# Kernel optimization log

Hardware: AMD Instinct MI355X
Metric: run time of the kernel (lower is better)

The kernel has to match this reference:

```python
import jax, jax.numpy as jnp
import numpy as np

C = 256
H_CH = 128  # channels // 2 (stage_index != 2)


def _gelu(x):
    # torch nn.GELU() default: exact erf formulation
    return jax.nn.gelu(x, approximate=False)


def _ln_channels(x, gamma, beta):
    # LayerNorm over channel dim (axis=1) of NCHW, eps=1e-5 (torch default)
    mu = jnp.mean(x, axis=1, keepdims=True)
    var = jnp.var(x, axis=1, keepdims=True)
    xn = (x - mu) * jax.lax.rsqrt(var + 1e-5)
    return xn * gamma[None, :, None, None] + beta[None, :, None, None]


def setup_inputs() -> dict:
    key = jax.random.key(0)
    ks = jax.random.split(key, 9)
    x = jax.random.normal(ks[0], (16, C, 64, 64), dtype=jnp.float32)
    s1 = 1.0 / np.sqrt(C)
    s2 = 1.0 / np.sqrt(H_CH)
    W1 = jax.random.uniform(ks[1], (H_CH, C), jnp.float32, -s1, s1)
    b1 = jax.random.uniform(ks[2], (H_CH,), jnp.float32, -s1, s1)
    g1 = jnp.ones((H_CH,), jnp.float32)
    be1 = jnp.zeros((H_CH,), jnp.float32)
    W2 = jax.random.uniform(ks[3], (C, H_CH), jnp.float32, -s2, s2)
    b2 = jax.random.uniform(ks[4], (C,), jnp.float32, -s2, s2)
    g2 = jnp.ones((C,), jnp.float32)
    be2 = jnp.zeros((C,), jnp.float32)
    return {"x": x, "W1": W1, "b1": b1, "g1": g1, "be1": be1,
            "W2": W2, "b2": b2, "g2": g2, "be2": be2}


def reference(x, W1, b1, g1, be1, W2, b2, g2, be2):
    identity = x
    # 1x1 conv == per-pixel channel matmul
    h = jnp.einsum('bchw,oc->bohw', x, W1) + b1[None, :, None, None]
    h = _gelu(_ln_channels(h, g1, be1))
    y = jnp.einsum('bchw,oc->bohw', h, W2) + b2[None, :, None, None]
    y = _ln_channels(y, g2, be2)
    return _gelu(y + identity)
```

## Files before the change

kernel.cpp:

```cpp
#include <hip/hip_runtime.h>

#define C_IN 256
#define HC   128
#define HW   4096

#define SX 260
#define SH 132
#define SO 68

typedef __attribute__((ext_vector_type(8))) short short8;
typedef __attribute__((ext_vector_type(4))) short short4v;
typedef __attribute__((ext_vector_type(4))) float f32x4;
typedef __attribute__((ext_vector_type(4))) unsigned short u16x4;

__device__ __forceinline__ unsigned short f2bf(float f) {
    union { float f; unsigned int u; } v; v.f = f;
    return (unsigned short)((v.u + 0x7FFFu + ((v.u >> 16) & 1u)) >> 16);
}

__device__ __forceinline__ float gelu_f(float v) {
    const float u = v * (0.7978845608028654f + 0.035677408136300125f * v * v);
    const float e = __expf(2.0f * u);
    const float t = 1.0f - 2.0f * __builtin_amdgcn_rcpf(e + 1.0f);
    return 0.5f * v * (1.0f + t);
}

__global__ void convert_weights(const float* __restrict__ W1, const float* __restrict__ W2,
                                unsigned short* __restrict__ W1b, unsigned short* __restrict__ W2b) {
    int i = blockIdx.x * blockDim.x + threadIdx.x;
    if (i < HC * C_IN) { W1b[i] = f2bf(W1[i]); W2b[i] = f2bf(W2[i]); }
}

union SmemU {
    unsigned short Xs[64 * SX];
    struct { unsigned short Hs[64 * SH]; float Ob[4][16][SO]; } u2;
};

template<bool USE_WS>
__global__ __launch_bounds__(256, 4) void fused_mlp(
    const float* __restrict__ x,
    const float* __restrict__ W1, const float* __restrict__ b1,
    const float* __restrict__ g1, const float* __restrict__ be1,
    const float* __restrict__ W2, const float* __restrict__ b2,
    const float* __restrict__ g2, const float* __restrict__ be2,
    const unsigned short* __restrict__ W1b, const unsigned short* __restrict__ W2b,
    float* __restrict__ out)
{
    __shared__ alignas(16) SmemU sm;
    __shared__ float red[4][64][2];

    const int tid = threadIdx.x;
    const int wv  = tid >> 6;
    const int l   = tid & 63;
    const int l15 = l & 15;
    const int kg  = l >> 4;

    const int tile = blockIdx.x;
    const int b    = tile >> 6;
    const int p0   = (tile & 63) * 64;
    const float* xb = x   + (size_t)b * (C_IN * HW) + p0;
    float*       ob = out + (size_t)b * (C_IN * HW) + p0;

    {
        const int g  = l15;
        const int cr = kg;
        #pragma unroll
        for (int rnd = 0; rnd < 4; ++rnd) {
            const int c0 = rnd * 64 + wv * 16 + cr * 4;
            f32x4 v[4];
            #pragma unroll
            for (int j = 0; j < 4; ++j)
                v[j] = *reinterpret_cast<const f32x4*>(xb + (size_t)(c0 + j) * HW + g * 4);
            #pragma unroll
            for (int jj = 0; jj < 4; ++jj) {
                u16x4 pk;
                #pragma unroll
                for (int j = 0; j < 4; ++j) pk[j] = f2bf(v[j][jj]);
                *reinterpret_cast<u16x4*>(&sm.Xs[(size_t)(g * 4 + jj) * SX + c0]) = pk;
            }
        }
    }
    __syncthreads();

    f32x4 acc1[2][4];
    const f32x4 vzero = {0.f, 0.f, 0.f, 0.f};
    #pragma unroll
    for (int mt = 0; mt < 2; ++mt)
        #pragma unroll
        for (int nt = 0; nt < 4; ++nt) acc1[mt][nt] = vzero;

    const int r0 = wv * 32;
    #pragma unroll
    for (int ks = 0; ks < 8; ++ks) {
        const int kb = ks * 32 + kg * 8;
        short8 a[2]; short4v blo[4], bhi[4];
        #pragma unroll
        for (int mt = 0; mt < 2; ++mt) {
            const int row = r0 + mt * 16 + l15;
            if constexpr (USE_WS) {
                a[mt] = *reinterpret_cast<const short8*>(W1b + (size_t)row * C_IN + kb);
            } else {
                const float* wp = W1 + (size_t)row * C_IN + kb;
                const f32x4 f0 = *reinterpret_cast<const f32x4*>(wp);
                const f32x4 f1 = *reinterpret_cast<const f32x4*>(wp + 4);
                #pragma unroll
                for (int e = 0; e < 4; ++e) { a[mt][e] = (short)f2bf(f0[e]); a[mt][4+e] = (short)f2bf(f1[e]); }
            }
        }
        #pragma unroll
        for (int nt = 0; nt < 4; ++nt) {
            const unsigned short* p = &sm.Xs[(size_t)(nt * 16 + l15) * SX + kb];
            blo[nt] = *reinterpret_cast<const short4v*>(p);
            bhi[nt] = *reinterpret_cast<const short4v*>(p + 4);
        }
        #pragma unroll
        for (int mt = 0; mt < 2; ++mt)
            #pragma unroll
            for (int nt = 0; nt < 4; ++nt) {
                const short8 bf = __builtin_shufflevector(blo[nt], bhi[nt], 0,1,2,3,4,5,6,7);
                acc1[mt][nt] = __builtin_amdgcn_mfma_f32_16x16x32_bf16(a[mt], bf, acc1[mt][nt], 0, 0, 0);
            }
    }

    #pragma unroll
    for (int mt = 0; mt < 2; ++mt) {
        const f32x4 bias = *reinterpret_cast<const f32x4*>(b1 + r0 + mt * 16 + kg * 4);
        #pragma unroll
        for (int nt = 0; nt < 4; ++nt) acc1[mt][nt] += bias;
    }
    #pragma unroll
    for (int nt = 0; nt < 4; ++nt) {
        float s = 0.f, q = 0.f;
        #pragma unroll
        for (int mt = 0; mt < 2; ++mt)
            #pragma unroll
            for (int r = 0; r < 4; ++r) { const float v = acc1[mt][nt][r]; s += v; q += v * v; }
        s += __shfl_xor(s, 16); s += __shfl_xor(s, 32);
        q += __shfl_xor(q, 16); q += __shfl_xor(q, 32);
        if (kg == 0) { red[wv][nt * 16 + l15][0] = s; red[wv][nt * 16 + l15][1] = q; }
    }
    __syncthreads();

    {
        f32x4 gm[2], bt[2];
        #pragma unroll
        for (int mt = 0; mt < 2; ++mt) {
            gm[mt] = *reinterpret_cast<const f32x4*>(g1  + r0 + mt * 16 + kg * 4);
            bt[mt] = *reinterpret_cast<const f32x4*>(be1 + r0 + mt * 16 + kg * 4);
        }
        #pragma unroll
        for (int nt = 0; nt < 4; ++nt) {
            const int col = nt * 16 + l15;
            float s = 0.f, q = 0.f;
            #pragma unroll
            for (int w2 = 0; w2 < 4; ++w2) { s += red[w2][col][0]; q += red[w2][col][1]; }
            const float mean = s * (1.0f / HC);
            const float rstd = rsqrtf(q * (1.0f / HC) - mean * mean + 1e-5f);
            #pragma unroll
            for (int mt = 0; mt < 2; ++mt) {
                u16x4 pk;
                #pragma unroll
                for (int r = 0; r < 4; ++r) {
                    float v = (acc1[mt][nt][r] - mean) * rstd;
                    v = v * gm[mt][r] + bt[mt][r];
                    pk[r] = f2bf(gelu_f(v));
                }
                *reinterpret_cast<u16x4*>(&sm.u2.Hs[(size_t)col * SH + r0 + mt * 16 + kg * 4]) = pk;
            }
        }
    }
    __syncthreads();

    f32x4 acc2[4][4];
    #pragma unroll
    for (int mt = 0; mt < 4; ++mt)
        #pragma unroll
        for (int nt = 0; nt < 4; ++nt) acc2[mt][nt] = vzero;

    const int r2 = wv * 64;
    #pragma unroll
    for (int ks = 0; ks < 4; ++ks) {
        const int kb = ks * 32 + kg * 8;
        short8 a[4]; short4v blo[4], bhi[4];
        #pragma unroll
        for (int mt = 0; mt < 4; ++mt) {
            const int row = r2 + mt * 16 + l15;
            if constexpr (USE_WS) {
                a[mt] = *reinterpret_cast<const short8*>(W2b + (size_t)row * HC + kb);
            } else {
                const float* wp = W2 + (size_t)row * HC + kb;
                const f32x4 f0 = *reinterpret_cast<const f32x4*>(wp);
                const f32x4 f1 = *reinterpret_cast<const f32x4*>(wp + 4);
                #pragma unroll
                for (int e = 0; e < 4; ++e) { a[mt][e] = (short)f2bf(f0[e]); a[mt][4+e] = (short)f2bf(f1[e]); }
            }
        }
        #pragma unroll
        for (int nt = 0; nt < 4; ++nt) {
            const unsigned short* p = &sm.u2.Hs[(size_t)(nt * 16 + l15) * SH + kb];
            blo[nt] = *reinterpret_cast<const short4v*>(p);
            bhi[nt] = *reinterpret_cast<const short4v*>(p + 4);
        }
        #pragma unroll
        for (int mt = 0; mt < 4; ++mt)
            #pragma unroll
            for (int nt = 0; nt < 4; ++nt) {
                const short8 bf = __builtin_shufflevector(blo[nt], bhi[nt], 0,1,2,3,4,5,6,7);
                acc2[mt][nt] = __builtin_amdgcn_mfma_f32_16x16x32_bf16(a[mt], bf, acc2[mt][nt], 0, 0, 0);
            }
    }

    #pragma unroll
    for (int mt = 0; mt < 4; ++mt) {
        const f32x4 bias = *reinterpret_cast<const f32x4*>(b2 + r2 + mt * 16 + kg * 4);
        #pragma unroll
        for (int nt = 0; nt < 4; ++nt) acc2[mt][nt] += bias;
    }
    #pragma unroll
    for (int nt = 0; nt < 4; ++nt) {
        float s = 0.f, q = 0.f;
        #pragma unroll
        for (int mt = 0; mt < 4; ++mt)
            #pragma unroll
            for (int r = 0; r < 4; ++r) { const float v = acc2[mt][nt][r]; s += v; q += v * v; }
        s += __shfl_xor(s, 16); s += __shfl_xor(s, 32);
        q += __shfl_xor(q, 16); q += __shfl_xor(q, 32);
        if (kg == 0) { red[wv][nt * 16 + l15][0] = s; red[wv][nt * 16 + l15][1] = q; }
    }
    __syncthreads();

    float mean2[4], rstd2[4];
    #pragma unroll
    for (int nt = 0; nt < 4; ++nt) {
        const int col = nt * 16 + l15;
        float s = 0.f, q = 0.f;
        #pragma unroll
        for (int w2 = 0; w2 < 4; ++w2) { s += red[w2][col][0]; q += red[w2][col][1]; }
        mean2[nt] = s * (1.0f / C_IN);
        rstd2[nt] = rsqrtf(q * (1.0f / C_IN) - mean2[nt] * mean2[nt] + 1e-5f);
    }

    #pragma unroll
    for (int mt = 0; mt < 4; ++mt) {
        const f32x4 gm = *reinterpret_cast<const f32x4*>(g2  + r2 + mt * 16 + kg * 4);
        const f32x4 bt = *reinterpret_cast<const f32x4*>(be2 + r2 + mt * 16 + kg * 4);
        #pragma unroll
        for (int nt = 0; nt < 4; ++nt) {
            #pragma unroll
            for (int r = 0; r < 4; ++r) {
                float v = (acc2[mt][nt][r] - mean2[nt]) * rstd2[nt];
                v = v * gm[r] + bt[r];
                sm.u2.Ob[wv][kg * 4 + r][nt * 16 + l15] = v;
            }
        }
        __syncthreads();
        #pragma unroll
        for (int m = 0; m < 4; ++m) {
            const int rl  = kg + 4 * m;
            const int row = r2 + mt * 16 + rl;
            const f32x4 y4 = *reinterpret_cast<const f32x4*>(&sm.u2.Ob[wv][rl][l15 * 4]);
            const f32x4 x4 = *reinterpret_cast<const f32x4*>(xb + (size_t)row * HW + l15 * 4);
            f32x4 o4;
            #pragma unroll
            for (int e = 0; e < 4; ++e) o4[e] = gelu_f(y4[e] + x4[e]);
            *reinterpret_cast<f32x4*>(ob + (size_t)row * HW + l15 * 4) = o4;
        }
        if (mt < 3) __syncthreads();
    }
}

extern "C" void kernel_launch(void* const* d_in, const int* in_sizes, int n_in,
                              void* d_out, int out_size, void* d_ws, size_t ws_size,
                              hipStream_t stream) {
    const float* x   = (const float*)d_in[0];
    const float* W1  = (const float*)d_in[1];
    const float* b1  = (const float*)d_in[2];
    const float* g1  = (const float*)d_in[3];
    const float* be1 = (const float*)d_in[4];
    const float* W2  = (const float*)d_in[5];
    const float* b2  = (const float*)d_in[6];
    const float* g2  = (const float*)d_in[7];
    const float* be2 = (const float*)d_in[8];
    float* out = (float*)d_out;

    const size_t need = (size_t)(HC * C_IN + C_IN * HC) * sizeof(unsigned short);
    if (ws_size >= need) {
        unsigned short* W1b = (unsigned short*)d_ws;
        unsigned short* W2b = W1b + HC * C_IN;
        convert_weights<<<128, 256, 0, stream>>>(W1, W2, W1b, W2b);
        fused_mlp<true><<<1024, 256, 0, stream>>>(x, W1, b1, g1, be1, W2, b2, g2, be2, W1b, W2b, out);
    } else {
        fused_mlp<false><<<1024, 256, 0, stream>>>(x, W1, b1, g1, be1, W2, b2, g2, be2, nullptr, nullptr, out);
    }
}
```

Measured before the change: 58.98 us.

## Halve pixel tile to 32, double grid, use per-wave LDS fences in epilogue

Shrinks each block's pixel tile from 64 to 32, doubling the grid to 2048 blocks and raising the launch-bounds occupancy target from 4 to 8 blocks per CU. LDS and accumulator register use drop accordingly. The second GEMM now loads W2 fragments in two halves to reduce live registers. The epilogue's block-wide barriers are replaced with wave-local LDS waitcnt fences, since each wave only touches its own Ob slice. The trade-off is that each W1/W2 fragment loaded is reused across half as many pixels, so per-pixel weight traffic rises.

```diff
diff --git a/kernel.cpp b/kernel.cpp
--- a/kernel.cpp
+++ b/kernel.cpp
@@ -3,10 +3,11 @@
 #define C_IN 256
 #define HC   128
 #define HW   4096
+#define TP   32
 
 #define SX 260
 #define SH 132
-#define SO 68
+#define SO 36
 
 typedef __attribute__((ext_vector_type(8))) short short8;
 typedef __attribute__((ext_vector_type(4))) short short4v;
@@ -25,6 +26,11 @@
     return 0.5f * v * (1.0f + t);
 }
 
+__device__ __forceinline__ void wave_lds_fence() {
+    asm volatile("s_waitcnt lgkmcnt(0)" ::: "memory");
+    __builtin_amdgcn_sched_barrier(0);
+}
+
 __global__ void convert_weights(const float* __restrict__ W1, const float* __restrict__ W2,
                                 unsigned short* __restrict__ W1b, unsigned short* __restrict__ W2b) {
     int i = blockIdx.x * blockDim.x + threadIdx.x;
@@ -32,12 +38,12 @@
 }
 
 union SmemU {
-    unsigned short Xs[64 * SX];
-    struct { unsigned short Hs[64 * SH]; float Ob[4][16][SO]; } u2;
+    unsigned short Xs[TP * SX];
+    struct { unsigned short Hs[TP * SH]; float Ob[4][16][SO]; } u2;
 };
 
 template<bool USE_WS>
-__global__ __launch_bounds__(256, 4) void fused_mlp(
+__global__ __launch_bounds__(256, 8) void fused_mlp(
     const float* __restrict__ x,
     const float* __restrict__ W1, const float* __restrict__ b1,
     const float* __restrict__ g1, const float* __restrict__ be1,
@@ -47,7 +53,7 @@
     float* __restrict__ out)
 {
     __shared__ alignas(16) SmemU sm;
-    __shared__ float red[4][64][2];
+    __shared__ float red[4][TP][2];
 
     const int tid = threadIdx.x;
     const int wv  = tid >> 6;
@@ -56,17 +62,17 @@
     const int kg  = l >> 4;
 
     const int tile = blockIdx.x;
-    const int b    = tile >> 6;
-    const int p0   = (tile & 63) * 64;
+    const int b    = tile >> 7;
+    const int p0   = (tile & 127) * TP;
     const float* xb = x   + (size_t)b * (C_IN * HW) + p0;
     float*       ob = out + (size_t)b * (C_IN * HW) + p0;
 
     {
-        const int g  = l15;
-        const int cr = kg;
-        #pragma unroll
-        for (int rnd = 0; rnd < 4; ++rnd) {
-            const int c0 = rnd * 64 + wv * 16 + cr * 4;
+        const int g  = tid & 7;
+        const int cq = tid >> 3;
+        #pragma unroll
+        for (int rnd = 0; rnd < 2; ++rnd) {
+            const int c0 = rnd * 128 + cq * 4;
             f32x4 v[4];
             #pragma unroll
             for (int j = 0; j < 4; ++j)
@@ -82,18 +88,18 @@
     }
     __syncthreads();
 
-    f32x4 acc1[2][4];
+    f32x4 acc1[2][2];
     const f32x4 vzero = {0.f, 0.f, 0.f, 0.f};
     #pragma unroll
     for (int mt = 0; mt < 2; ++mt)
         #pragma unroll
-        for (int nt = 0; nt < 4; ++nt) acc1[mt][nt] = vzero;
+        for (int nt = 0; nt < 2; ++nt) acc1[mt][nt] = vzero;
 
     const int r0 = wv * 32;
     #pragma unroll
     for (int ks = 0; ks < 8; ++ks) {
         const int kb = ks * 32 + kg * 8;
-        short8 a[2]; short4v blo[4], bhi[4];
+        short8 a[2]; short4v blo[2], bhi[2];
         #pragma unroll
         for (int mt = 0; mt < 2; ++mt) {
             const int row = r0 + mt * 16 + l15;
@@ -108,7 +114,7 @@
             }
         }
         #pragma unroll
-        for (int nt = 0; nt < 4; ++nt) {
+        for (int nt = 0; nt < 2; ++nt) {
             const unsigned short* p = &sm.Xs[(size_t)(nt * 16 + l15) * SX + kb];
             blo[nt] = *reinterpret_cast<const short4v*>(p);
             bhi[nt] = *reinterpret_cast<const short4v*>(p + 4);
@@ -116,7 +122,7 @@
         #pragma unroll
         for (int mt = 0; mt < 2; ++mt)
             #pragma unroll
-            for (int nt = 0; nt < 4; ++nt) {
+            for (int nt = 0; nt < 2; ++nt) {
                 const short8 bf = __builtin_shufflevector(blo[nt], bhi[nt], 0,1,2,3,4,5,6,7);
                 acc1[mt][nt] = __builtin_amdgcn_mfma_f32_16x16x32_bf16(a[mt], bf, acc1[mt][nt], 0, 0, 0);
             }
@@ -126,10 +132,10 @@
     for (int mt = 0; mt < 2; ++mt) {
         const f32x4 bias = *reinterpret_cast<const f32x4*>(b1 + r0 + mt * 16 + kg * 4);
         #pragma unroll
-        for (int nt = 0; nt < 4; ++nt) acc1[mt][nt] += bias;
-    }
-    #pragma unroll
-    for (int nt = 0; nt < 4; ++nt) {
+        for (int nt = 0; nt < 2; ++nt) acc1[mt][nt] += bias;
+    }
+    #pragma unroll
+    for (int nt = 0; nt < 2; ++nt) {
         float s = 0.f, q = 0.f;
         #pragma unroll
         for (int mt = 0; mt < 2; ++mt)
@@ -149,7 +155,7 @@
             bt[mt] = *reinterpret_cast<const f32x4*>(be1 + r0 + mt * 16 + kg * 4);
         }
         #pragma unroll
-        for (int nt = 0; nt < 4; ++nt) {
+        for (int nt = 0; nt < 2; ++nt) {
             const int col = nt * 16 + l15;
             float s = 0.f, q = 0.f;
             #pragma unroll
@@ -171,53 +177,57 @@
     }
     __syncthreads();
 
-    f32x4 acc2[4][4];
+    f32x4 acc2[4][2];
     #pragma unroll
     for (int mt = 0; mt < 4; ++mt)
         #pragma unroll
-        for (int nt = 0; nt < 4; ++nt) acc2[mt][nt] = vzero;
+        for (int nt = 0; nt < 2; ++nt) acc2[mt][nt] = vzero;
 
     const int r2 = wv * 64;
     #pragma unroll
     for (int ks = 0; ks < 4; ++ks) {
         const int kb = ks * 32 + kg * 8;
-        short8 a[4]; short4v blo[4], bhi[4];
-        #pragma unroll
-        for (int mt = 0; mt < 4; ++mt) {
-            const int row = r2 + mt * 16 + l15;
-            if constexpr (USE_WS) {
-                a[mt] = *reinterpret_cast<const short8*>(W2b + (size_t)row * HC + kb);
-            } else {
-                const float* wp = W2 + (size_t)row * HC + kb;
-                const f32x4 f0 = *reinterpret_cast<const f32x4*>(wp);
-                const f32x4 f1 = *reinterpret_cast<const f32x4*>(wp + 4);
-                #pragma unroll
-                for (int e = 0; e < 4; ++e) { a[mt][e] = (short)f2bf(f0[e]); a[mt][4+e] = (short)f2bf(f1[e]); }
-            }
-        }
-        #pragma unroll
-        for (int nt = 0; nt < 4; ++nt) {
+        short4v blo[2], bhi[2];
+        #pragma unroll
+        for (int nt = 0; nt < 2; ++nt) {
             const unsigned short* p = &sm.u2.Hs[(size_t)(nt * 16 + l15) * SH + kb];
             blo[nt] = *reinterpret_cast<const short4v*>(p);
             bhi[nt] = *reinterpret_cast<const short4v*>(p + 4);
         }
         #pragma unroll
-        for (int mt = 0; mt < 4; ++mt)
-            #pragma unroll
-            for (int nt = 0; nt < 4; ++nt) {
-                const short8 bf = __builtin_shufflevector(blo[nt], bhi[nt], 0,1,2,3,4,5,6,7);
-                acc2[mt][nt] = __builtin_amdgcn_mfma_f32_16x16x32_bf16(a[mt], bf, acc2[mt][nt], 0, 0, 0);
-            }
+        for (int half = 0; half < 2; ++half) {
+            short8 a[2];
+            #pragma unroll
+            for (int m2 = 0; m2 < 2; ++m2) {
+                const int row = r2 + (half * 2 + m2) * 16 + l15;
+                if constexpr (USE_WS) {
+                    a[m2] = *reinterpret_cast<const short8*>(W2b + (size_t)row * HC + kb);
+                } else {
+                    const float* wp = W2 + (size_t)row * HC + kb;
+                    const f32x4 f0 = *reinterpret_cast<const f32x4*>(wp);
+                    const f32x4 f1 = *reinterpret_cast<const f32x4*>(wp + 4);
+                    #pragma unroll
+                    for (int e = 0; e < 4; ++e) { a[m2][e] = (short)f2bf(f0[e]); a[m2][4+e] = (short)f2bf(f1[e]); }
+                }
+            }
+            #pragma unroll
+            for (int m2 = 0; m2 < 2; ++m2)
+                #pragma unroll
+                for (int nt = 0; nt < 2; ++nt) {
+                    const short8 bf = __builtin_shufflevector(blo[nt], bhi[nt], 0,1,2,3,4,5,6,7);
+                    acc2[half * 2 + m2][nt] = __builtin_amdgcn_mfma_f32_16x16x32_bf16(a[m2], bf, acc2[half * 2 + m2][nt], 0, 0, 0);
+                }
+        }
     }
 
     #pragma unroll
     for (int mt = 0; mt < 4; ++mt) {
         const f32x4 bias = *reinterpret_cast<const f32x4*>(b2 + r2 + mt * 16 + kg * 4);
         #pragma unroll
-        for (int nt = 0; nt < 4; ++nt) acc2[mt][nt] += bias;
-    }
-    #pragma unroll
-    for (int nt = 0; nt < 4; ++nt) {
+        for (int nt = 0; nt < 2; ++nt) acc2[mt][nt] += bias;
+    }
+    #pragma unroll
+    for (int nt = 0; nt < 2; ++nt) {
         float s = 0.f, q = 0.f;
         #pragma unroll
         for (int mt = 0; mt < 4; ++mt)
@@ -229,9 +239,9 @@
     }
     __syncthreads();
 
-    float mean2[4], rstd2[4];
-    #pragma unroll
-    for (int nt = 0; nt < 4; ++nt) {
+    float mean2[2], rstd2[2];
+    #pragma unroll
+    for (int nt = 0; nt < 2; ++nt) {
         const int col = nt * 16 + l15;
         float s = 0.f, q = 0.f;
         #pragma unroll
@@ -245,7 +255,7 @@
         const f32x4 gm = *reinterpret_cast<const f32x4*>(g2  + r2 + mt * 16 + kg * 4);
         const f32x4 bt = *reinterpret_cast<const f32x4*>(be2 + r2 + mt * 16 + kg * 4);
         #pragma unroll
-        for (int nt = 0; nt < 4; ++nt) {
+        for (int nt = 0; nt < 2; ++nt) {
             #pragma unroll
             for (int r = 0; r < 4; ++r) {
                 float v = (acc2[mt][nt][r] - mean2[nt]) * rstd2[nt];
@@ -253,19 +263,20 @@
                 sm.u2.Ob[wv][kg * 4 + r][nt * 16 + l15] = v;
             }
         }
-        __syncthreads();
-        #pragma unroll
-        for (int m = 0; m < 4; ++m) {
-            const int rl  = kg + 4 * m;
+        wave_lds_fence();
+        #pragma unroll
+        for (int m = 0; m < 2; ++m) {
+            const int rl  = (l >> 3) + 8 * m;
+            const int cq4 = (l & 7) * 4;
             const int row = r2 + mt * 16 + rl;
-            const f32x4 y4 = *reinterpret_cast<const f32x4*>(&sm.u2.Ob[wv][rl][l15 * 4]);
-            const f32x4 x4 = *reinterpret_cast<const f32x4*>(xb + (size_t)row * HW + l15 * 4);
+            const f32x4 y4 = *reinterpret_cast<const f32x4*>(&sm.u2.Ob[wv][rl][cq4]);
+            const f32x4 x4 = *reinterpret_cast<const f32x4*>(xb + (size_t)row * HW + cq4);
             f32x4 o4;
             #pragma unroll
             for (int e = 0; e < 4; ++e) o4[e] = gelu_f(y4[e] + x4[e]);
-            *reinterpret_cast<f32x4*>(ob + (size_t)row * HW + l15 * 4) = o4;
-        }
-        if (mt < 3) __syncthreads();
+            *reinterpret_cast<f32x4*>(ob + (size_t)row * HW + cq4) = o4;
+        }
+        if (mt < 3) wave_lds_fence();
     }
 }
 
@@ -288,8 +299,8 @@
         unsigned short* W1b = (unsigned short*)d_ws;
         unsigned short* W2b = W1b + HC * C_IN;
         convert_weights<<<128, 256, 0, stream>>>(W1, W2, W1b, W2b);
-        fused_mlp<true><<<1024, 256, 0, stream>>>(x, W1, b1, g1, be1, W2, b2, g2, be2, W1b, W2b, out);
+        fused_mlp<true><<<2048, 256, 0, stream>>>(x, W1, b1, g1, be1, W2, b2, g2, be2, W1b, W2b, out);
     } else {
-        fused_mlp<false><<<1024, 256, 0, stream>>>(x, W1, b1, g1, be1, W2, b2, g2, be2, nullptr, nullptr, out);
-    }
-}
+        fused_mlp<false><<<2048, 256, 0, stream>>>(x, W1, b1, g1, be1, W2, b2, g2, be2, nullptr, nullptr, out);
+    }
+}
```

Result: slower. 69.68 us (+18.1%).

## Split x staging across GEMM1 halves, prefetch residual, replace block barriers with wave fences

Applied to the files above, without the earlier changes.

The x tile load is split so the second half of channels is loaded early and converted to LDS after the first half of GEMM1, overlapping global loads with MFMA work. Residual x rows for the epilogue are prefetched before GEMM2 and one step ahead in each epilogue iteration. The per-wave output staging buffer now uses only an lgkmcnt wait instead of a full __syncthreads, since each wave owns its own slice. W2 fragment loads are split into halves to reduce register pressure, and gelu switches to exp2f. Holding more data in registers may raise VGPR use and lower occupancy.

```diff
diff --git a/kernel.cpp b/kernel.cpp
--- a/kernel.cpp
+++ b/kernel.cpp
@@ -3,6 +3,7 @@
 #define C_IN 256
 #define HC   128
 #define HW   4096
+#define TP   64
 
 #define SX 260
 #define SH 132
@@ -11,6 +12,7 @@
 typedef __attribute__((ext_vector_type(8))) short short8;
 typedef __attribute__((ext_vector_type(4))) short short4v;
 typedef __attribute__((ext_vector_type(4))) float f32x4;
+typedef __attribute__((ext_vector_type(2))) float f32x2;
 typedef __attribute__((ext_vector_type(4))) unsigned short u16x4;
 
 __device__ __forceinline__ unsigned short f2bf(float f) {
@@ -20,9 +22,20 @@
 
 __device__ __forceinline__ float gelu_f(float v) {
     const float u = v * (0.7978845608028654f + 0.035677408136300125f * v * v);
-    const float e = __expf(2.0f * u);
+    const float e = exp2f(u * 2.8853900817779268f);
     const float t = 1.0f - 2.0f * __builtin_amdgcn_rcpf(e + 1.0f);
     return 0.5f * v * (1.0f + t);
+}
+
+__device__ __forceinline__ void block_sync() {
+    asm volatile("s_waitcnt lgkmcnt(0)" ::: "memory");
+    __builtin_amdgcn_s_barrier();
+    asm volatile("" ::: "memory");
+    __builtin_amdgcn_sched_barrier(0);
+}
+
+__device__ __forceinline__ void wave_lds_fence() {
+    asm volatile("s_waitcnt lgkmcnt(0)" ::: "memory");
 }
 
 __global__ void convert_weights(const float* __restrict__ W1, const float* __restrict__ W2,
@@ -32,8 +45,8 @@
 }
 
 union SmemU {
-    unsigned short Xs[64 * SX];
-    struct { unsigned short Hs[64 * SH]; float Ob[4][16][SO]; } u2;
+    unsigned short Xs[TP * SX];
+    struct { unsigned short Hs[TP * SH]; float Ob[4][16][SO]; } u2;
 };
 
 template<bool USE_WS>
@@ -47,7 +60,7 @@
     float* __restrict__ out)
 {
     __shared__ alignas(16) SmemU sm;
-    __shared__ float red[4][64][2];
+    __shared__ float red[4][TP][2];
 
     const int tid = threadIdx.x;
     const int wv  = tid >> 6;
@@ -55,32 +68,37 @@
     const int l15 = l & 15;
     const int kg  = l >> 4;
 
-    const int tile = blockIdx.x;
-    const int b    = tile >> 6;
-    const int p0   = (tile & 63) * 64;
+    const int bid = blockIdx.x;
+    const int b   = bid >> 6;
+    const int p0  = (bid & 63) * TP;
     const float* xb = x   + (size_t)b * (C_IN * HW) + p0;
     float*       ob = out + (size_t)b * (C_IN * HW) + p0;
 
-    {
-        const int g  = l15;
-        const int cr = kg;
-        #pragma unroll
-        for (int rnd = 0; rnd < 4; ++rnd) {
-            const int c0 = rnd * 64 + wv * 16 + cr * 4;
-            f32x4 v[4];
-            #pragma unroll
-            for (int j = 0; j < 4; ++j)
-                v[j] = *reinterpret_cast<const f32x4*>(xb + (size_t)(c0 + j) * HW + g * 4);
-            #pragma unroll
-            for (int jj = 0; jj < 4; ++jj) {
-                u16x4 pk;
-                #pragma unroll
-                for (int j = 0; j < 4; ++j) pk[j] = f2bf(v[j][jj]);
-                *reinterpret_cast<u16x4*>(&sm.Xs[(size_t)(g * 4 + jj) * SX + c0]) = pk;
-            }
-        }
-    }
-    __syncthreads();
+    const int g  = l15;
+    const int cs = wv * 16 + kg * 4;
+    f32x4 v0[8], v1[8];
+    #pragma unroll
+    for (int rnd = 0; rnd < 2; ++rnd)
+        #pragma unroll
+        for (int j = 0; j < 4; ++j)
+            v0[rnd * 4 + j] = *reinterpret_cast<const f32x4*>(xb + (size_t)(rnd * 64 + cs + j) * HW + g * 4);
+    #pragma unroll
+    for (int rnd = 0; rnd < 2; ++rnd)
+        #pragma unroll
+        for (int j = 0; j < 4; ++j)
+            v1[rnd * 4 + j] = *reinterpret_cast<const f32x4*>(xb + (size_t)((rnd + 2) * 64 + cs + j) * HW + g * 4);
+    #pragma unroll
+    for (int rnd = 0; rnd < 2; ++rnd) {
+        const int c0 = rnd * 64 + cs;
+        #pragma unroll
+        for (int jj = 0; jj < 4; ++jj) {
+            u16x4 pk;
+            #pragma unroll
+            for (int j = 0; j < 4; ++j) pk[j] = f2bf(v0[rnd * 4 + j][jj]);
+            *reinterpret_cast<u16x4*>(&sm.Xs[(size_t)(g * 4 + jj) * SX + c0]) = pk;
+        }
+    }
+    block_sync();
 
     f32x4 acc1[2][4];
     const f32x4 vzero = {0.f, 0.f, 0.f, 0.f};
@@ -91,7 +109,7 @@
 
     const int r0 = wv * 32;
     #pragma unroll
-    for (int ks = 0; ks < 8; ++ks) {
+    for (int ks = 0; ks < 4; ++ks) {
         const int kb = ks * 32 + kg * 8;
         short8 a[2]; short4v blo[4], bhi[4];
         #pragma unroll
@@ -123,6 +141,51 @@
     }
 
     #pragma unroll
+    for (int rnd = 0; rnd < 2; ++rnd) {
+        const int c0 = (rnd + 2) * 64 + cs;
+        #pragma unroll
+        for (int jj = 0; jj < 4; ++jj) {
+            u16x4 pk;
+            #pragma unroll
+            for (int j = 0; j < 4; ++j) pk[j] = f2bf(v1[rnd * 4 + j][jj]);
+            *reinterpret_cast<u16x4*>(&sm.Xs[(size_t)(g * 4 + jj) * SX + c0]) = pk;
+        }
+    }
+    block_sync();
+
+    #pragma unroll
+    for (int ks = 4; ks < 8; ++ks) {
+        const int kb = ks * 32 + kg * 8;
+        short8 a[2]; short4v blo[4], bhi[4];
+        #pragma unroll
+        for (int mt = 0; mt < 2; ++mt) {
+            const int row = r0 + mt * 16 + l15;
+            if constexpr (USE_WS) {
+                a[mt] = *reinterpret_cast<const short8*>(W1b + (size_t)row * C_IN + kb);
+            } else {
+                const float* wp = W1 + (size_t)row * C_IN + kb;
+                const f32x4 f0 = *reinterpret_cast<const f32x4*>(wp);
+                const f32x4 f1 = *reinterpret_cast<const f32x4*>(wp + 4);
+                #pragma unroll
+                for (int e = 0; e < 4; ++e) { a[mt][e] = (short)f2bf(f0[e]); a[mt][4+e] = (short)f2bf(f1[e]); }
+            }
+        }
+        #pragma unroll
+        for (int nt = 0; nt < 4; ++nt) {
+            const unsigned short* p = &sm.Xs[(size_t)(nt * 16 + l15) * SX + kb];
+            blo[nt] = *reinterpret_cast<const short4v*>(p);
+            bhi[nt] = *reinterpret_cast<const short4v*>(p + 4);
+        }
+        #pragma unroll
+        for (int mt = 0; mt < 2; ++mt)
+            #pragma unroll
+            for (int nt = 0; nt < 4; ++nt) {
+                const short8 bf = __builtin_shufflevector(blo[nt], bhi[nt], 0,1,2,3,4,5,6,7);
+                acc1[mt][nt] = __builtin_amdgcn_mfma_f32_16x16x32_bf16(a[mt], bf, acc1[mt][nt], 0, 0, 0);
+            }
+    }
+
+    #pragma unroll
     for (int mt = 0; mt < 2; ++mt) {
         const f32x4 bias = *reinterpret_cast<const f32x4*>(b1 + r0 + mt * 16 + kg * 4);
         #pragma unroll
@@ -139,7 +202,7 @@
         q += __shfl_xor(q, 16); q += __shfl_xor(q, 32);
         if (kg == 0) { red[wv][nt * 16 + l15][0] = s; red[wv][nt * 16 + l15][1] = q; }
     }
-    __syncthreads();
+    block_sync();
 
     {
         f32x4 gm[2], bt[2];
@@ -169,7 +232,13 @@
             }
         }
     }
-    __syncthreads();
+    block_sync();
+
+    const int r2 = wv * 64;
+    f32x4 xp[4];
+    #pragma unroll
+    for (int m = 0; m < 4; ++m)
+        xp[m] = *reinterpret_cast<const f32x4*>(xb + (size_t)(r2 + kg + 4 * m) * HW + l15 * 4);
 
     f32x4 acc2[4][4];
     #pragma unroll
@@ -177,24 +246,10 @@
         #pragma unroll
         for (int nt = 0; nt < 4; ++nt) acc2[mt][nt] = vzero;
 
-    const int r2 = wv * 64;
     #pragma unroll
     for (int ks = 0; ks < 4; ++ks) {
         const int kb = ks * 32 + kg * 8;
-        short8 a[4]; short4v blo[4], bhi[4];
-        #pragma unroll
-        for (int mt = 0; mt < 4; ++mt) {
-            const int row = r2 + mt * 16 + l15;
-            if constexpr (USE_WS) {
-                a[mt] = *reinterpret_cast<const short8*>(W2b + (size_t)row * HC + kb);
-            } else {
-                const float* wp = W2 + (size_t)row * HC + kb;
-                const f32x4 f0 = *reinterpret_cast<const f32x4*>(wp);
-                const f32x4 f1 = *reinterpret_cast<const f32x4*>(wp + 4);
-                #pragma unroll
-                for (int e = 0; e < 4; ++e) { a[mt][e] = (short)f2bf(f0[e]); a[mt][4+e] = (short)f2bf(f1[e]); }
-            }
-        }
+        short4v blo[4], bhi[4];
         #pragma unroll
         for (int nt = 0; nt < 4; ++nt) {
             const unsigned short* p = &sm.u2.Hs[(size_t)(nt * 16 + l15) * SH + kb];
@@ -202,12 +257,29 @@
             bhi[nt] = *reinterpret_cast<const short4v*>(p + 4);
         }
         #pragma unroll
-        for (int mt = 0; mt < 4; ++mt)
-            #pragma unroll
-            for (int nt = 0; nt < 4; ++nt) {
-                const short8 bf = __builtin_shufflevector(blo[nt], bhi[nt], 0,1,2,3,4,5,6,7);
-                acc2[mt][nt] = __builtin_amdgcn_mfma_f32_16x16x32_bf16(a[mt], bf, acc2[mt][nt], 0, 0, 0);
-            }
+        for (int half = 0; half < 2; ++half) {
+            short8 a[2];
+            #pragma unroll
+            for (int m2 = 0; m2 < 2; ++m2) {
+                const int row = r2 + (half * 2 + m2) * 16 + l15;
+                if constexpr (USE_WS) {
+                    a[m2] = *reinterpret_cast<const short8*>(W2b + (size_t)row * HC + kb);
+                } else {
+                    const float* wp = W2 + (size_t)row * HC + kb;
+                    const f32x4 f0 = *reinterpret_cast<const f32x4*>(wp);
+                    const f32x4 f1 = *reinterpret_cast<const f32x4*>(wp + 4);
+                    #pragma unroll
+                    for (int e = 0; e < 4; ++e) { a[m2][e] = (short)f2bf(f0[e]); a[m2][4+e] = (short)f2bf(f1[e]); }
+                }
+            }
+            #pragma unroll
+            for (int m2 = 0; m2 < 2; ++m2)
+                #pragma unroll
+                for (int nt = 0; nt < 4; ++nt) {
+                    const short8 bf = __builtin_shufflevector(blo[nt], bhi[nt], 0,1,2,3,4,5,6,7);
+                    acc2[half * 2 + m2][nt] = __builtin_amdgcn_mfma_f32_16x16x32_bf16(a[m2], bf, acc2[half * 2 + m2][nt], 0, 0, 0);
+                }
+        }
     }
 
     #pragma unroll
@@ -227,7 +299,7 @@
         q += __shfl_xor(q, 16); q += __shfl_xor(q, 32);
         if (kg == 0) { red[wv][nt * 16 + l15][0] = s; red[wv][nt * 16 + l15][1] = q; }
     }
-    __syncthreads();
+    block_sync();
 
     float mean2[4], rstd2[4];
     #pragma unroll
@@ -253,19 +325,30 @@
                 sm.u2.Ob[wv][kg * 4 + r][nt * 16 + l15] = v;
             }
         }
-        __syncthreads();
+        f32x4 xn[4];
+        if (mt < 3) {
+            #pragma unroll
+            for (int m = 0; m < 4; ++m)
+                xn[m] = *reinterpret_cast<const f32x4*>(xb + (size_t)(r2 + (mt + 1) * 16 + kg + 4 * m) * HW + l15 * 4);
+        }
+        wave_lds_fence();
         #pragma unroll
         for (int m = 0; m < 4; ++m) {
             const int rl  = kg + 4 * m;
             const int row = r2 + mt * 16 + rl;
-            const f32x4 y4 = *reinterpret_cast<const f32x4*>(&sm.u2.Ob[wv][rl][l15 * 4]);
-            const f32x4 x4 = *reinterpret_cast<const f32x4*>(xb + (size_t)row * HW + l15 * 4);
+            const float* op = &sm.u2.Ob[wv][rl][l15 * 4];
+            const f32x2 ylo = *reinterpret_cast<const f32x2*>(op);
+            const f32x2 yhi = *reinterpret_cast<const f32x2*>(op + 2);
             f32x4 o4;
-            #pragma unroll
-            for (int e = 0; e < 4; ++e) o4[e] = gelu_f(y4[e] + x4[e]);
+            o4[0] = gelu_f(ylo[0] + xp[m][0]);
+            o4[1] = gelu_f(ylo[1] + xp[m][1]);
+            o4[2] = gelu_f(yhi[0] + xp[m][2]);
+            o4[3] = gelu_f(yhi[1] + xp[m][3]);
             *reinterpret_cast<f32x4*>(ob + (size_t)row * HW + l15 * 4) = o4;
         }
-        if (mt < 3) __syncthreads();
+        #pragma unroll
+        for (int m = 0; m < 4; ++m) xp[m] = xn[m];
+        if (mt < 3) wave_lds_fence();
     }
 }
 
```

After: 57.97 us (median of 2 runs). About the same (-1.7%).
